# Performance work log

Hardware: AMD Instinct MI355X
Metric: run time of the kernel (lower is better)

## Reference

```python
import jax, jax.numpy as jnp
import numpy as np

N = 65536   # total goals in library
D = 256     # flattened embedding dim
B = 2048    # batch_size (last B entries are the new batch)


def setup_inputs() -> dict:
    key = jax.random.key(0)
    k1, k2 = jax.random.split(key)
    return {
        "target_lib": jax.random.normal(k1, (N, D), dtype=jnp.float32),
        "reached_lib": jax.random.normal(k2, (N, D), dtype=jnp.float32),
        "batch_size": B,
    }


def _euclid(a, b):
    # distance_fn: Euclidean distance between two embeddings
    return jnp.sqrt(jnp.sum((a - b) ** 2))


def _nearest_idx(queries, lib):
    # top-1 nearest neighbor via squared-distance expansion (same argmin as cdist)
    qn = jnp.sum(queries * queries, axis=1, keepdims=True)      # [B,1]
    ln = jnp.sum(lib * lib, axis=1)                             # [L]
    d2 = qn + ln[None, :] - 2.0 * (queries @ lib.T)             # [B,L]
    return jnp.argmin(d2, axis=1)                               # [B]


def reference(target_lib, reached_lib, batch_size):
    targets = target_lib[-batch_size:]          # [B,D] newest target goals
    reached = reached_lib[-batch_size:]         # [B,D] newest reached goals
    prev = reached_lib[:-batch_size]            # [N-B,D] previously reached goals

    prev_closest = prev[_nearest_idx(targets, prev)]       # [B,D]
    new_closest = reached[_nearest_idx(targets, reached)]  # [B,D]

    def LP(t, init_e, reached_e):
        return _euclid(t, init_e) - _euclid(t, reached_e)

    IM_vals, IM_grads = jax.vmap(jax.value_and_grad(LP, 0))(
        targets, prev_closest, new_closest)
    return IM_vals, IM_grads
```

## Files before the change

kernel.cpp:

```cpp
#include <hip/hip_runtime.h>
#include <math.h>

#define NTOT   65536
#define DDIM   256
#define BATCH  2048
#define NPREV  (NTOT - BATCH)

#define PWP    62
#define PWR    32
#define UPC_P  16
#define UPC_R  1
#define BNC_P  31
#define BNC_R  16

#define INF_F 3.402823466e+38f
#define SWZ(r) ((((r) & 3)) ^ ((((r) >> 2) & 3)))

typedef float  f32x4  __attribute__((ext_vector_type(4)));
typedef float  f32x16 __attribute__((ext_vector_type(16)));
typedef _Float16 half8 __attribute__((ext_vector_type(8)));

#define TILE_HALVES 65536

#define SCHED_FENCE() __builtin_amdgcn_sched_barrier(0)
#define RAW_BARRIER() do { SCHED_FENCE(); __builtin_amdgcn_s_barrier(); SCHED_FENCE(); } while (0)
#define VMCNT2()  do { asm volatile("s_waitcnt vmcnt(2)" ::: "memory"); SCHED_FENCE(); } while (0)
#define VMCNT0()  do { asm volatile("s_waitcnt vmcnt(0)" ::: "memory"); SCHED_FENCE(); } while (0)

__global__ void lp_norms(const float* __restrict__ lib, float* __restrict__ ln) {
    const int row  = blockIdx.x * 4 + (threadIdx.x >> 6);
    const int lane = threadIdx.x & 63;
    const float4 v = reinterpret_cast<const float4*>(lib + (size_t)row * DDIM)[lane];
    float s = v.x * v.x + v.y * v.y + v.z * v.z + v.w * v.w;
#pragma unroll
    for (int off = 32; off > 0; off >>= 1) s += __shfl_down(s, off);
    if (lane == 0) ln[row] = s;
}

__device__ __forceinline__ void cvt_split(const f32x4 a, const f32x4 b,
                                          half8& h, half8& l) {
    float v[8] = {a[0], a[1], a[2], a[3], b[0], b[1], b[2], b[3]};
#pragma unroll
    for (int j = 0; j < 8; ++j) {
        const float s = v[j] * 256.0f;
        const _Float16 hh = (_Float16)s;
        const _Float16 ll = (_Float16)(s - (float)hh);
        h[j] = hh; l[j] = ll;
    }
}

__global__ void lp_split32(const float* __restrict__ src, _Float16* __restrict__ dst,
                           float* __restrict__ ln) {
    const int tile = blockIdx.x;
    const int t    = threadIdx.x;
    const int rg   = t >> 6;
    const int l    = t & 63;
    const int row  = rg * 32 + (l & 31);
    const int k8   = l >> 5;
    const float* srcR = src + (size_t)tile * 128 * DDIM + (size_t)row * DDIM;
    _Float16*    dstT = dst + (size_t)tile * TILE_HALVES;

    float nsum = 0.f;
#pragma unroll
    for (int kb = 0; kb < 8; ++kb) {
#pragma unroll
        for (int kk = 0; kk < 2; ++kk) {
            const float* p = srcR + kb * 32 + kk * 16 + k8 * 8;
            const f32x4 a = *reinterpret_cast<const f32x4*>(p);
            const f32x4 b = *reinterpret_cast<const f32x4*>(p + 4);
            half8 h, lo; cvt_split(a, b, h, lo);
            const size_t off = ((size_t)(((kb * 2 + 0) * 4 + rg) * 2 + kk) * 64 + l) * 8;
            *reinterpret_cast<half8*>(dstT + off)        = h;
            *reinterpret_cast<half8*>(dstT + off + 4096) = lo;
            nsum += a[0]*a[0] + a[1]*a[1] + a[2]*a[2] + a[3]*a[3]
                  + b[0]*b[0] + b[1]*b[1] + b[2]*b[2] + b[3]*b[3];
        }
    }
    nsum += __shfl_xor(nsum, 32);
    if (ln != nullptr && k8 == 0) ln[(size_t)tile * 128 + row] = nsum;
}

__device__ __forceinline__ void gload16(const _Float16* g, _Float16* lds) {
    __builtin_amdgcn_global_load_lds(
        (const __attribute__((address_space(1))) void*)g,
        (__attribute__((address_space(3))) void*)lds, 16, 0, 0);
}

__global__ __launch_bounds__(256, 2)
void lp_nn_mfma9(const _Float16* __restrict__ Qs, const _Float16* __restrict__ Ls,
                 const float* __restrict__ ln, int unitsPC, int nchunks,
                 float* __restrict__ pscore, int* __restrict__ pidx)
{
    __shared__ _Float16 LB[2][4096];
    __shared__ float lnLds[1024];

    const int nwg  = 16 * nchunks;
    const int hid  = blockIdx.x;
    const int work = (hid & 7) * (nwg >> 3) + (hid >> 3);
    const int bx   = work & 15;
    const int by   = work >> 4;

    const int t    = threadIdx.x;
    const int lane = t & 63;
    const int wid  = t >> 6;
    const int col  = lane & 31, hi = lane >> 5;

    const _Float16* Qt = Qs + (size_t)bx * TILE_HALVES;
    const int u0    = by * unitsPC;
    const int NSTEP = unitsPC * 8;

    half8 qf[8][2][2];
#pragma unroll
    for (int kb = 0; kb < 8; ++kb)
#pragma unroll
        for (int hl = 0; hl < 2; ++hl)
#pragma unroll
            for (int kk = 0; kk < 2; ++kk)
                qf[kb][hl][kk] = *reinterpret_cast<const half8*>(
                    Qt + ((((kb * 2 + hl) * 4 + wid) * 2) + kk) * 512 + lane * 8);

    auto stageL = [&](int buf, int s) {
        const int u = u0 + (s >> 3), kb = s & 7;
        const int tile = u >> 1, half = u & 1;
        const _Float16* base = Ls + (size_t)tile * TILE_HALVES;
#pragma unroll
        for (int hl = 0; hl < 2; ++hl)
            gload16(base + ((kb * 2 + hl) * 4 + half * 2) * 1024 + t * 8,
                    &LB[buf][hl * 2048 + wid * 512]);
    };

    {
        const float* lsrc = ln + (size_t)u0 * 64;
        __builtin_amdgcn_global_load_lds(
            (const __attribute__((address_space(1))) void*)(lsrc + t * 4),
            (__attribute__((address_space(3))) void*)(&lnLds[wid * 256]),
            16, 0, 0);
    }
    stageL(0, 0);
    stageL(1, 1);

    float bkey[16];
    int   bidxr[16];
    f32x16 acc[2];
#pragma unroll
    for (int r = 0; r < 16; ++r) { bkey[r] = INF_F; bidxr[r] = 0x7fffffff; }
    acc[0] = (f32x16)(0.f); acc[1] = (f32x16)(0.f);

    float lnv0 = 0.f, lnv1 = 0.f;

    for (int un = 0; un < unitsPC; ++un) {
#pragma unroll
        for (int kb = 0; kb < 8; ++kb) {
            const int s = un * 8 + kb;
            if (s == NSTEP - 1) VMCNT0(); else VMCNT2();
            RAW_BARRIER();
            if (kb == 0) {
                lnv0 = lnLds[un * 64 + col];
                lnv1 = lnLds[un * 64 + 32 + col];
            }
            const _Float16* B = LB[s & 1];
            half8 bf[2][2][2];
#pragma unroll
            for (int nf = 0; nf < 2; ++nf)
#pragma unroll
                for (int hl = 0; hl < 2; ++hl)
#pragma unroll
                    for (int kk = 0; kk < 2; ++kk)
                        bf[nf][hl][kk] = *reinterpret_cast<const half8*>(
                            B + hl * 2048 + nf * 1024 + kk * 512 + lane * 8);
            __builtin_amdgcn_s_setprio(1);
#pragma unroll
            for (int kk = 0; kk < 2; ++kk)
#pragma unroll
                for (int term = 0; term < 3; ++term) {
                    const int ta = (term == 2) ? 1 : 0;
                    const int tb = (term == 1) ? 1 : 0;
                    acc[0] = __builtin_amdgcn_mfma_f32_32x32x16_f16(
                        qf[kb][ta][kk], bf[0][tb][kk], acc[0], 0, 0, 0);
                    acc[1] = __builtin_amdgcn_mfma_f32_32x32x16_f16(
                        qf[kb][ta][kk], bf[1][tb][kk], acc[1], 0, 0, 0);
                }
            __builtin_amdgcn_s_setprio(0);
            RAW_BARRIER();
            if (s + 2 < NSTEP) stageL(s & 1, s + 2);
        }
        const int u = u0 + un;
#pragma unroll
        for (int nf = 0; nf < 2; ++nf) {
            const int gidx = u * 64 + nf * 32 + col;
            const float lnvs = (nf ? lnv1 : lnv0) * 65536.0f;
#pragma unroll
            for (int r = 0; r < 16; ++r) {
                const float key = fmaf(-2.f, acc[nf][r], lnvs);
                if (key < bkey[r] || (key == bkey[r] && gidx < bidxr[r])) {
                    bkey[r] = key; bidxr[r] = gidx;
                }
                acc[nf][r] = 0.f;
            }
        }
    }

#pragma unroll
    for (int off = 1; off < 32; off <<= 1)
#pragma unroll
        for (int r = 0; r < 16; ++r) {
            const float ok = __shfl_xor(bkey[r], off);
            const int   oi = __shfl_xor(bidxr[r], off);
            if (ok < bkey[r] || (ok == bkey[r] && oi < bidxr[r])) {
                bkey[r] = ok; bidxr[r] = oi;
            }
        }
    if (col == 0)
#pragma unroll
        for (int r = 0; r < 16; ++r) {
            const int q = bx * 128 + wid * 32 + (r & 3) + 8 * (r >> 2) + 4 * hi;
            pscore[(size_t)q * nchunks + by] = bkey[r];
            pidx  [(size_t)q * nchunks + by] = bidxr[r];
        }
}

__global__ __launch_bounds__(256, 2)
void lp_nn_mfma_fb(const float* __restrict__ Q, const float* __restrict__ L,
                   const float* __restrict__ ln, int chunkRows,
                   float* __restrict__ pscore, int* __restrict__ pidx, int nchunks)
{
    __shared__ _Float16 Ah[128 * 32];
    __shared__ _Float16 Al[128 * 32];
    __shared__ _Float16 Bh[128 * 32];
    __shared__ _Float16 Bl[128 * 32];
    __shared__ float xk[2][128];
    __shared__ int   xi[2][128];

    const int t    = threadIdx.x;
    const int wid  = t >> 6, lane = t & 63;
    const int wq   = wid >> 1, wl = wid & 1;
    const int col  = lane & 15, rg = lane >> 4;
    const int qbase = blockIdx.x * 128;
    const int chunkBase = blockIdx.y * chunkRows;
    const int srow   = t >> 2;
    const int schunk = t & 3;

    float bkey[4][4];
    int   bidxr[4][4];
#pragma unroll
    for (int mf = 0; mf < 4; ++mf)
#pragma unroll
        for (int i = 0; i < 4; ++i) { bkey[mf][i] = INF_F; bidxr[mf][i] = 0x7fffffff; }

    for (int lt = 0; lt < chunkRows; lt += 128) {
        f32x4 acc[4][4];
#pragma unroll
        for (int mf = 0; mf < 4; ++mf)
#pragma unroll
            for (int nf = 0; nf < 4; ++nf) acc[mf][nf] = (f32x4)(0.f);

        for (int kb = 0; kb < DDIM; kb += 32) {
            __syncthreads();
#pragma unroll
            for (int sr = 0; sr < 2; ++sr) {
                const int r = srow + 64 * sr;
                const int s = schunk ^ SWZ(r);
                {
                    const float* src = Q + (size_t)(qbase + r) * DDIM + kb + schunk * 8;
                    const f32x4 a = *reinterpret_cast<const f32x4*>(src);
                    const f32x4 b = *reinterpret_cast<const f32x4*>(src + 4);
                    half8 h, l; cvt_split(a, b, h, l);
                    *reinterpret_cast<half8*>(&Ah[r * 32 + s * 8]) = h;
                    *reinterpret_cast<half8*>(&Al[r * 32 + s * 8]) = l;
                }
                {
                    const float* src = L + (size_t)(chunkBase + lt + r) * DDIM + kb + schunk * 8;
                    const f32x4 a = *reinterpret_cast<const f32x4*>(src);
                    const f32x4 b = *reinterpret_cast<const f32x4*>(src + 4);
                    half8 h, l; cvt_split(a, b, h, l);
                    *reinterpret_cast<half8*>(&Bh[r * 32 + s * 8]) = h;
                    *reinterpret_cast<half8*>(&Bl[r * 32 + s * 8]) = l;
                }
            }
            __syncthreads();

            half8 ah[4], al[4];
#pragma unroll
            for (int mf = 0; mf < 4; ++mf) {
                const int r = wq * 64 + mf * 16 + col;
                const int s = rg ^ SWZ(r);
                ah[mf] = *reinterpret_cast<const half8*>(&Ah[r * 32 + s * 8]);
                al[mf] = *reinterpret_cast<const half8*>(&Al[r * 32 + s * 8]);
            }
#pragma unroll
            for (int nf = 0; nf < 4; ++nf) {
                const int r = wl * 64 + nf * 16 + col;
                const int s = rg ^ SWZ(r);
                const half8 bh = *reinterpret_cast<const half8*>(&Bh[r * 32 + s * 8]);
                const half8 bl = *reinterpret_cast<const half8*>(&Bl[r * 32 + s * 8]);
#pragma unroll
                for (int mf = 0; mf < 4; ++mf) {
                    acc[mf][nf] = __builtin_amdgcn_mfma_f32_16x16x32_f16(ah[mf], bh, acc[mf][nf], 0, 0, 0);
                    acc[mf][nf] = __builtin_amdgcn_mfma_f32_16x16x32_f16(ah[mf], bl, acc[mf][nf], 0, 0, 0);
                    acc[mf][nf] = __builtin_amdgcn_mfma_f32_16x16x32_f16(al[mf], bh, acc[mf][nf], 0, 0, 0);
                }
            }
        }

#pragma unroll
        for (int nf = 0; nf < 4; ++nf) {
            const int gidx = chunkBase + lt + wl * 64 + nf * 16 + col;
            const float lnv = ln[gidx] * 65536.0f;
#pragma unroll
            for (int mf = 0; mf < 4; ++mf)
#pragma unroll
                for (int i = 0; i < 4; ++i) {
                    const float key = fmaf(-2.f, acc[mf][nf][i], lnv);
                    if (key < bkey[mf][i] || (key == bkey[mf][i] && gidx < bidxr[mf][i])) {
                        bkey[mf][i] = key; bidxr[mf][i] = gidx;
                    }
                }
        }
    }

#pragma unroll
    for (int off = 1; off < 16; off <<= 1)
#pragma unroll
        for (int mf = 0; mf < 4; ++mf)
#pragma unroll
            for (int i = 0; i < 4; ++i) {
                const float ok = __shfl_xor(bkey[mf][i], off);
                const int   oi = __shfl_xor(bidxr[mf][i], off);
                if (ok < bkey[mf][i] || (ok == bkey[mf][i] && oi < bidxr[mf][i])) {
                    bkey[mf][i] = ok; bidxr[mf][i] = oi;
                }
            }
    if (col == 0)
#pragma unroll
        for (int mf = 0; mf < 4; ++mf)
#pragma unroll
            for (int i = 0; i < 4; ++i) {
                const int ql = wq * 64 + mf * 16 + rg * 4 + i;
                xk[wl][ql] = bkey[mf][i];
                xi[wl][ql] = bidxr[mf][i];
            }
    __syncthreads();
    if (t < 128) {
        float bk = xk[0][t]; int bi = xi[0][t];
        const float k2 = xk[1][t]; const int i2 = xi[1][t];
        if (k2 < bk || (k2 == bk && i2 < bi)) { bk = k2; bi = i2; }
        const int q = qbase + t;
        pscore[(size_t)q * nchunks + blockIdx.y] = bk;
        pidx  [(size_t)q * nchunks + blockIdx.y] = bi;
    }
}

__global__ void lp_finalize(const float* __restrict__ Q,
                            const float* __restrict__ prevL,
                            const float* __restrict__ reachL,
                            const float* __restrict__ ps_p, const int* __restrict__ pi_p,
                            const float* __restrict__ ps_r, const int* __restrict__ pi_r,
                            int ncp, int ncr,
                            float* __restrict__ out)
{
    const int q = blockIdx.x;
    const int lane = threadIdx.x;

    float k1 = (lane < ncp) ? ps_p[(size_t)q * ncp + lane] : INF_F;
    int   i1 = (lane < ncp) ? pi_p[(size_t)q * ncp + lane] : 0x7fffffff;
#pragma unroll
    for (int off = 32; off > 0; off >>= 1) {
        const float ok = __shfl_xor(k1, off);
        const int   oi = __shfl_xor(i1, off);
        if (ok < k1 || (ok == k1 && oi < i1)) { k1 = ok; i1 = oi; }
    }
    float k2 = (lane < ncr) ? ps_r[(size_t)q * ncr + lane] : INF_F;
    int   i2 = (lane < ncr) ? pi_r[(size_t)q * ncr + lane] : 0x7fffffff;
#pragma unroll
    for (int off = 32; off > 0; off >>= 1) {
        const float ok = __shfl_xor(k2, off);
        const int   oi = __shfl_xor(i2, off);
        if (ok < k2 || (ok == k2 && oi < i2)) { k2 = ok; i2 = oi; }
    }

    const float4 tv = reinterpret_cast<const float4*>(Q      + (size_t)q  * DDIM)[lane];
    const float4 e1 = reinterpret_cast<const float4*>(prevL  + (size_t)i1 * DDIM)[lane];
    const float4 e2 = reinterpret_cast<const float4*>(reachL + (size_t)i2 * DDIM)[lane];
    const float4 d1 = {tv.x - e1.x, tv.y - e1.y, tv.z - e1.z, tv.w - e1.w};
    const float4 d2 = {tv.x - e2.x, tv.y - e2.y, tv.z - e2.z, tv.w - e2.w};
    float s1 = d1.x * d1.x + d1.y * d1.y + d1.z * d1.z + d1.w * d1.w;
    float s2 = d2.x * d2.x + d2.y * d2.y + d2.z * d2.z + d2.w * d2.w;
#pragma unroll
    for (int off = 32; off > 0; off >>= 1) {
        s1 += __shfl_xor(s1, off);
        s2 += __shfl_xor(s2, off);
    }
    const float r1 = sqrtf(s1), r2 = sqrtf(s2);
    float4 g;
    g.x = d1.x / r1 - d2.x / r2;
    g.y = d1.y / r1 - d2.y / r2;
    g.z = d1.z / r1 - d2.z / r2;
    g.w = d1.w / r1 - d2.w / r2;
    reinterpret_cast<float4*>(out + BATCH + (size_t)q * DDIM)[lane] = g;
    if (lane == 0) out[q] = r1 - r2;
}

extern "C" void kernel_launch(void* const* d_in, const int* in_sizes, int n_in,
                              void* d_out, int out_size, void* d_ws, size_t ws_size,
                              hipStream_t stream) {
    const float* target_lib  = (const float*)d_in[0];
    const float* reached_lib = (const float*)d_in[1];
    const float* Qp     = target_lib  + (size_t)NPREV * DDIM;
    const float* prevL  = reached_lib;
    const float* reachL = reached_lib + (size_t)NPREV * DDIM;

    float* ws     = (float*)d_ws;
    float* ln_all = ws;
    float* ps_p   = ln_all + NTOT;
    float* ps_r   = ps_p + (size_t)BATCH * PWP;
    int*   pi_p   = (int*)(ps_r + (size_t)BATCH * PWR);
    int*   pi_r   = pi_p + (size_t)BATCH * PWP;
    _Float16* Qsp = (_Float16*)(pi_r + (size_t)BATCH * PWR);
    _Float16* Lsp = Qsp + (size_t)(BATCH / 128) * TILE_HALVES;
    float* out    = (float*)d_out;

    const size_t need = (size_t)(NTOT + 2 * BATCH * (PWP + PWR)) * 4
                      + (size_t)(BATCH / 128 + NTOT / 128) * TILE_HALVES * 2;

    if (ws_size >= need) {
        lp_split32<<<NTOT / 128, 256, 0, stream>>>(reached_lib, Lsp, ln_all);
        lp_split32<<<BATCH / 128, 256, 0, stream>>>(Qp, Qsp, nullptr);
        lp_nn_mfma9<<<16 * PWP, 256, 0, stream>>>(
            Qsp, Lsp, ln_all, UPC_P, PWP, ps_p, pi_p);
        lp_nn_mfma9<<<16 * PWR, 256, 0, stream>>>(
            Qsp, Lsp + (size_t)(NPREV / 128) * TILE_HALVES,
            ln_all + NPREV, UPC_R, PWR, ps_r, pi_r);
        lp_finalize<<<BATCH, 64, 0, stream>>>(
            Qp, prevL, reachL, ps_p, pi_p, ps_r, pi_r, PWP, PWR, out);
    } else {
        lp_norms<<<NTOT / 4, 256, 0, stream>>>(reached_lib, ln_all);
        lp_nn_mfma_fb<<<dim3(BATCH / 128, BNC_P), 256, 0, stream>>>(
            Qp, prevL, ln_all, 2048, ps_p, pi_p, BNC_P);
        lp_nn_mfma_fb<<<dim3(BATCH / 128, BNC_R), 256, 0, stream>>>(
            Qp, reachL, ln_all + NPREV, 128, ps_r, pi_r, BNC_R);
        lp_finalize<<<BATCH, 64, 0, stream>>>(
            Qp, prevL, reachL, ps_p, pi_p, ps_r, pi_r, BNC_P, BNC_R, out);
    }
}
```

Before: 250.0 us.

## Triple-buffer library tiles and prefetch LDS fragments into registers

Replaces the double-buffered LDS staging with a three-slot ring, so each step issues the next global-to-LDS load before waiting and needs one barrier per step instead of two. It also reads the next step's B fragments from LDS into a second register set while the current MFMAs run, overlapping LDS reads with matrix math. The partition of the previous-goal library changes from 62 chunks of 16 units to 32 chunks of 31 units, which halves the workgroup count and doubles the lnLds buffer. The extra register set and LDS slot may lower occupancy, and fewer, longer workgroups change load balance across CUs.

```diff
diff --git a/kernel.cpp b/kernel.cpp
--- a/kernel.cpp
+++ b/kernel.cpp
@@ -6,9 +6,9 @@
 #define BATCH  2048
 #define NPREV  (NTOT - BATCH)
 
-#define PWP    62
+#define PWP    32
 #define PWR    32
-#define UPC_P  16
+#define UPC_P  31
 #define UPC_R  1
 #define BNC_P  31
 #define BNC_R  16
@@ -26,6 +26,7 @@
 #define RAW_BARRIER() do { SCHED_FENCE(); __builtin_amdgcn_s_barrier(); SCHED_FENCE(); } while (0)
 #define VMCNT2()  do { asm volatile("s_waitcnt vmcnt(2)" ::: "memory"); SCHED_FENCE(); } while (0)
 #define VMCNT0()  do { asm volatile("s_waitcnt vmcnt(0)" ::: "memory"); SCHED_FENCE(); } while (0)
+#define LGKM0()   do { asm volatile("s_waitcnt lgkmcnt(0)" ::: "memory"); SCHED_FENCE(); } while (0)
 
 __global__ void lp_norms(const float* __restrict__ lib, float* __restrict__ ln) {
     const int row  = blockIdx.x * 4 + (threadIdx.x >> 6);
@@ -86,13 +87,46 @@
         (__attribute__((address_space(3))) void*)lds, 16, 0, 0);
 }
 
+#define NN_STEP(kb_, RC, RN, STAGE_OK, VM, READ_OK)                              \
+  {                                                                              \
+    const int s_ = un * 8 + (kb_);                                               \
+    if (STAGE_OK) stageL((s_ + 2) % 3, s_ + 2);                                  \
+    VM;                                                                          \
+    RAW_BARRIER();                                                               \
+    LGKM0();                                                                     \
+    __builtin_amdgcn_s_setprio(1);                                               \
+    _Pragma("unroll")                                                            \
+    for (int kk = 0; kk < 2; ++kk)                                               \
+      _Pragma("unroll")                                                          \
+      for (int term = 0; term < 3; ++term) {                                     \
+        const int ta = (term == 2) ? 1 : 0;                                      \
+        const int tb = (term == 1) ? 1 : 0;                                      \
+        acc[0] = __builtin_amdgcn_mfma_f32_32x32x16_f16(                         \
+            qf[kb_][ta][kk], RC[0][tb][kk], acc[0], 0, 0, 0);                    \
+        acc[1] = __builtin_amdgcn_mfma_f32_32x32x16_f16(                         \
+            qf[kb_][ta][kk], RC[1][tb][kk], acc[1], 0, 0, 0);                    \
+      }                                                                          \
+    __builtin_amdgcn_s_setprio(0);                                               \
+    if (READ_OK) {                                                               \
+      const _Float16* Bn = &LB[(s_ + 1) % 3][0];                                 \
+      _Pragma("unroll")                                                          \
+      for (int nf = 0; nf < 2; ++nf)                                             \
+        _Pragma("unroll")                                                        \
+        for (int hl = 0; hl < 2; ++hl)                                           \
+          _Pragma("unroll")                                                      \
+          for (int kk = 0; kk < 2; ++kk)                                         \
+            RN[nf][hl][kk] = *reinterpret_cast<const half8*>(                    \
+                Bn + hl * 2048 + nf * 1024 + kk * 512 + lane * 8);               \
+    }                                                                            \
+  }
+
 __global__ __launch_bounds__(256, 2)
-void lp_nn_mfma9(const _Float16* __restrict__ Qs, const _Float16* __restrict__ Ls,
-                 const float* __restrict__ ln, int unitsPC, int nchunks,
-                 float* __restrict__ pscore, int* __restrict__ pidx)
+void lp_nn_mfma10(const _Float16* __restrict__ Qs, const _Float16* __restrict__ Ls,
+                  const float* __restrict__ ln, int unitsPC, int nchunks,
+                  float* __restrict__ pscore, int* __restrict__ pidx)
 {
-    __shared__ _Float16 LB[2][4096];
-    __shared__ float lnLds[1024];
+    __shared__ _Float16 LB[3][4096];
+    __shared__ float lnLds[2048];
 
     const int nwg  = 16 * nchunks;
     const int hid  = blockIdx.x;
@@ -129,16 +163,6 @@
                     &LB[buf][hl * 2048 + wid * 512]);
     };
 
-    {
-        const float* lsrc = ln + (size_t)u0 * 64;
-        __builtin_amdgcn_global_load_lds(
-            (const __attribute__((address_space(1))) void*)(lsrc + t * 4),
-            (__attribute__((address_space(3))) void*)(&lnLds[wid * 256]),
-            16, 0, 0);
-    }
-    stageL(0, 0);
-    stageL(1, 1);
-
     float bkey[16];
     int   bidxr[16];
     f32x16 acc[2];
@@ -146,45 +170,10 @@
     for (int r = 0; r < 16; ++r) { bkey[r] = INF_F; bidxr[r] = 0x7fffffff; }
     acc[0] = (f32x16)(0.f); acc[1] = (f32x16)(0.f);
 
-    float lnv0 = 0.f, lnv1 = 0.f;
-
-    for (int un = 0; un < unitsPC; ++un) {
-#pragma unroll
-        for (int kb = 0; kb < 8; ++kb) {
-            const int s = un * 8 + kb;
-            if (s == NSTEP - 1) VMCNT0(); else VMCNT2();
-            RAW_BARRIER();
-            if (kb == 0) {
-                lnv0 = lnLds[un * 64 + col];
-                lnv1 = lnLds[un * 64 + 32 + col];
-            }
-            const _Float16* B = LB[s & 1];
-            half8 bf[2][2][2];
-#pragma unroll
-            for (int nf = 0; nf < 2; ++nf)
-#pragma unroll
-                for (int hl = 0; hl < 2; ++hl)
-#pragma unroll
-                    for (int kk = 0; kk < 2; ++kk)
-                        bf[nf][hl][kk] = *reinterpret_cast<const half8*>(
-                            B + hl * 2048 + nf * 1024 + kk * 512 + lane * 8);
-            __builtin_amdgcn_s_setprio(1);
-#pragma unroll
-            for (int kk = 0; kk < 2; ++kk)
-#pragma unroll
-                for (int term = 0; term < 3; ++term) {
-                    const int ta = (term == 2) ? 1 : 0;
-                    const int tb = (term == 1) ? 1 : 0;
-                    acc[0] = __builtin_amdgcn_mfma_f32_32x32x16_f16(
-                        qf[kb][ta][kk], bf[0][tb][kk], acc[0], 0, 0, 0);
-                    acc[1] = __builtin_amdgcn_mfma_f32_32x32x16_f16(
-                        qf[kb][ta][kk], bf[1][tb][kk], acc[1], 0, 0, 0);
-                }
-            __builtin_amdgcn_s_setprio(0);
-            RAW_BARRIER();
-            if (s + 2 < NSTEP) stageL(s & 1, s + 2);
-        }
+    auto fold = [&](int un) {
         const int u = u0 + un;
+        const float lnv0 = lnLds[un * 64 + col];
+        const float lnv1 = lnLds[un * 64 + 32 + col];
 #pragma unroll
         for (int nf = 0; nf < 2; ++nf) {
             const int gidx = u * 64 + nf * 32 + col;
@@ -198,6 +187,54 @@
                 acc[nf][r] = 0.f;
             }
         }
+    };
+
+    {
+        const float* lsrc = ln + (size_t)u0 * 64;
+#pragma unroll
+        for (int j = 0; j < 2; ++j)
+            __builtin_amdgcn_global_load_lds(
+                (const __attribute__((address_space(1))) void*)(lsrc + j * 1024 + t * 4),
+                (__attribute__((address_space(3))) void*)(&lnLds[j * 1024 + wid * 256]),
+                16, 0, 0);
+    }
+    stageL(0, 0);
+    stageL(1, 1);
+    VMCNT2();
+    RAW_BARRIER();
+
+    half8 bfA[2][2][2], bfB[2][2][2];
+#pragma unroll
+    for (int nf = 0; nf < 2; ++nf)
+#pragma unroll
+        for (int hl = 0; hl < 2; ++hl)
+#pragma unroll
+            for (int kk = 0; kk < 2; ++kk)
+                bfA[nf][hl][kk] = *reinterpret_cast<const half8*>(
+                    &LB[0][0] + hl * 2048 + nf * 1024 + kk * 512 + lane * 8);
+
+    for (int un = 0; un < unitsPC - 1; ++un) {
+        NN_STEP(0, bfA, bfB, true, VMCNT2(), true)
+        NN_STEP(1, bfB, bfA, true, VMCNT2(), true)
+        NN_STEP(2, bfA, bfB, true, VMCNT2(), true)
+        NN_STEP(3, bfB, bfA, true, VMCNT2(), true)
+        NN_STEP(4, bfA, bfB, true, VMCNT2(), true)
+        NN_STEP(5, bfB, bfA, true, VMCNT2(), true)
+        NN_STEP(6, bfA, bfB, true, VMCNT2(), true)
+        NN_STEP(7, bfB, bfA, true, VMCNT2(), true)
+        fold(un);
+    }
+    {
+        const int un = unitsPC - 1;
+        NN_STEP(0, bfA, bfB, true,  VMCNT2(), true)
+        NN_STEP(1, bfB, bfA, true,  VMCNT2(), true)
+        NN_STEP(2, bfA, bfB, true,  VMCNT2(), true)
+        NN_STEP(3, bfB, bfA, true,  VMCNT2(), true)
+        NN_STEP(4, bfA, bfB, true,  VMCNT2(), true)
+        NN_STEP(5, bfB, bfA, true,  VMCNT2(), true)
+        NN_STEP(6, bfA, bfB, false, VMCNT0(), true)
+        NN_STEP(7, bfB, bfA, false, VMCNT0(), false)
+        fold(un);
     }
 
 #pragma unroll
@@ -425,9 +462,9 @@
     if (ws_size >= need) {
         lp_split32<<<NTOT / 128, 256, 0, stream>>>(reached_lib, Lsp, ln_all);
         lp_split32<<<BATCH / 128, 256, 0, stream>>>(Qp, Qsp, nullptr);
-        lp_nn_mfma9<<<16 * PWP, 256, 0, stream>>>(
+        lp_nn_mfma10<<<16 * PWP, 256, 0, stream>>>(
             Qsp, Lsp, ln_all, UPC_P, PWP, ps_p, pi_p);
-        lp_nn_mfma9<<<16 * PWR, 256, 0, stream>>>(
+        lp_nn_mfma10<<<16 * PWR, 256, 0, stream>>>(
             Qsp, Lsp + (size_t)(NPREV / 128) * TILE_HALVES,
             ln_all + NPREV, UPC_R, PWR, ps_r, pi_r);
         lp_finalize<<<BATCH, 64, 0, stream>>>(
```

After: 237.0 us. 1.05x faster.
